# Kernel tuning notes

Hardware: AMD Instinct MI355X
Metric: run time of the kernel (lower is better)

The kernel has to match this reference:

```python
import math
import jax, jax.numpy as jnp
import numpy as np

B, S, D, H = 2, 2048, 1024, 16
DH = D // H


def setup_inputs() -> dict:
    key = jax.random.key(0)
    ks = jax.random.split(key, 12)
    s = 1.0 / math.sqrt(D)
    return {
        "x_q": jax.random.normal(ks[0], (B, S, D), jnp.float32),
        "x_k": jax.random.normal(ks[1], (B, S, D), jnp.float32),
        "x_v": jax.random.normal(ks[2], (B, S, D), jnp.float32),
        "mask": jax.random.randint(ks[3], (B, S), 0, 2) > 0,
        "Wq": jax.random.normal(ks[4], (D, D), jnp.float32) * s,
        "bq": jnp.zeros((D,), jnp.float32),
        "Wk": jax.random.normal(ks[5], (D, D), jnp.float32) * s,
        "bk": jnp.zeros((D,), jnp.float32),
        "Wv": jax.random.normal(ks[6], (D, D), jnp.float32) * s,
        "bv": jnp.zeros((D,), jnp.float32),
        "Wo": jax.random.normal(ks[7], (D, D), jnp.float32) * s,
        "bo": jnp.zeros((D,), jnp.float32),
    }


def reference(x_q, x_k, x_v, mask, Wq, bq, Wk, bk, Wv, bv, Wo, bo):
    # nn.Linear: y = x @ W^T + b
    Q = jnp.einsum('bsd,ed->bse', x_q, Wq) + bq
    K = jnp.einsum('bsd,ed->bse', x_k, Wk) + bk
    V = jnp.einsum('bsd,ed->bse', x_v, Wv) + bv
    b, sq, d = Q.shape
    # split(dim_split, 2) + cat(dim=0) == per-head attention on [B,S,H,DH]
    Qh = Q.reshape(b, sq, H, DH)
    Kh = K.reshape(b, -1, H, DH)
    Vh = V.reshape(b, -1, H, DH)
    scores = jnp.einsum('bqhd,bkhd->bhqk', Qh, Kh) / math.sqrt(DH)
    # inf_mask: -1e9 where mask is False, broadcast over heads and queries
    scores = scores + jnp.where(mask[:, None, None, :], 0.0, -1e9)
    A = jax.nn.softmax(scores, axis=-1)  # dropout is identity in eval
    out = jnp.einsum('bhqk,bkhd->bqhd', A, Vh).reshape(b, sq, d)
    return jnp.einsum('bsd,ed->bse', out, Wo) + bo
```

## Files before the change

### kernel.cpp

```cpp
#include <hip/hip_runtime.h>
#include <hip/hip_bf16.h>
#include <stdint.h>

#define BB  2
#define SS  2048
#define DDIM 1024
#define HH  16
#define DH  64

typedef __attribute__((ext_vector_type(8))) short short8;
typedef __attribute__((ext_vector_type(4))) short short4v;
typedef __attribute__((ext_vector_type(4))) float float4v;

#define AS1 __attribute__((address_space(1)))
#define AS3 __attribute__((address_space(3)))

static __device__ __forceinline__ void gl2lds16(const void* g, void* l) {
  __builtin_amdgcn_global_load_lds((const AS1 unsigned int*)g,
                                   (AS3 unsigned int*)l, 16, 0, 0);
}

static __device__ __forceinline__ float bf2f(short s) {
  union { unsigned u; float f; } c;
  c.u = ((unsigned)(unsigned short)s) << 16;
  return c.f;
}
static __device__ __forceinline__ short f2bf(float f) {
  union { float ff; unsigned u; } c;
  c.ff = f;
  unsigned u = c.u;
  u += 0x7fffu + ((u >> 16) & 1u);
  return (short)(u >> 16);
}

static __device__ __forceinline__ unsigned cvtpk(float x, float y) {
  union { __hip_bfloat162 h; unsigned u; } c;
  c.h = __float22bfloat162_rn(float2{x, y});
  return c.u;
}

#if __has_builtin(__builtin_amdgcn_exp2f)
static __device__ __forceinline__ float exp2fast(float x) { return __builtin_amdgcn_exp2f(x); }
#else
static __device__ __forceinline__ float exp2fast(float x) { return __expf(x * 0.69314718056f); }
#endif

static __device__ __forceinline__ int detect_f32(const void* p) {
  const float* f = (const float*)p;
  int ok = 1;
#pragma unroll
  for (int i = 0; i < 16; i++) {
    float a = fabsf(f[i]);
    ok &= (a > 1e-10f && a < 1e4f) ? 1 : 0;
  }
  return ok;
}

struct CvtArgs {
  const void* xq; const void* xk; const void* xv;
  const void* wq; const void* wk; const void* wv; const void* wo;
  const void* b0; const void* b1; const void* b2; const void* b3;
  const int* mask;
  short* dst;
  float* mw;
};

__global__ __launch_bounds__(256)
void cvt_kernel(CvtArgs a) {
  const int f32m = detect_f32(a.xq);
  const size_t gtid = (size_t)blockIdx.x * blockDim.x + threadIdx.x;
  const size_t stride = (size_t)gridDim.x * blockDim.x;
  const size_t M4 = (size_t)4 << 20, M1 = (size_t)1 << 20, TOT = (size_t)16 << 20;
  for (size_t i = gtid; i * 4 < TOT; i += stride) {
    const size_t idx = i * 4;
    const void* src;
    size_t off;
    if (idx < 3 * M4) {
      size_t xi = idx / M4;
      off = idx & (M4 - 1);
      src = (xi == 0) ? a.xq : (xi == 1) ? a.xk : a.xv;
    } else {
      size_t wi = (idx - 3 * M4) / M1;
      off = idx & (M1 - 1);
      src = (wi == 0) ? a.wq : (wi == 1) ? a.wk : (wi == 2) ? a.wv : a.wo;
    }
    short4v o;
    if (f32m) {
      float4v v = *(const float4v*)((const float*)src + off);
      union { unsigned u[2]; short4v s; } pk;
      pk.u[0] = cvtpk(v[0], v[1]);
      pk.u[1] = cvtpk(v[2], v[3]);
      o = pk.s;
    } else {
      o = *(const short4v*)((const short*)src + off);
    }
    *(short4v*)(a.dst + idx) = o;
  }
  if (gtid < 1024) {
    const void* bs[4] = {a.b0, a.b1, a.b2, a.b3};
#pragma unroll
    for (int j = 0; j < 4; j++) {
      short v = f32m ? f2bf(((const float*)bs[j])[gtid])
                     : ((const short*)bs[j])[gtid];
      a.dst[TOT + (size_t)j * 1024 + gtid] = v;
    }
  }
  if (gtid < BB * SS)
    a.mw[gtid] = a.mask[gtid] ? -23.083120654223414f : -1e9f;
}

struct GemmArgs {
  const short* x[3];
  const short* w[3];
  const short* b[3];
  short* o[3];
  const void* probe;
  int tmask;
  int detect_out;
};

template <int MW>
__global__ __launch_bounds__(256)
void gemm_kernel(GemmArgs a) {
  constexpr int GK = 1024, GN = 1024;
  __shared__ alignas(16) short As[32 * MW * 32];
  __shared__ alignas(16) short Bs[128 * 32];

  const int t = threadIdx.x;
  const int w = t >> 6, l = t & 63, l15 = l & 15, qd = l >> 4;
  const int bn = blockIdx.x, bm = blockIdx.y, mat = blockIdx.z;

  const short* X  = a.x[mat];
  const short* W  = a.w[mat];
  const short* Bi = a.b[mat];
  short* O        = a.o[mat];
  const int transposed = (a.tmask >> mat) & 1;

  const short* Ag = X + (size_t)bm * (32 * MW) * GK;
  const short* Bg = W + (size_t)bn * 128 * GK;

  const int L0 = t, L1 = 256 + t;
  const int r0 = L0 >> 2, g0 = (L0 & 3) ^ ((r0 >> 1) & 3);
  const int r1 = L1 >> 2, g1 = (L1 & 3) ^ ((r1 >> 1) & 3);
  const size_t off0 = (size_t)r0 * GK + g0 * 8;
  const size_t off1 = (size_t)r1 * GK + g1 * 8;

  float4v acc[MW][4];
#pragma unroll
  for (int i = 0; i < MW; i++)
#pragma unroll
    for (int j = 0; j < 4; j++) acc[i][j] = (float4v){0.f, 0.f, 0.f, 0.f};

  const int wm = (w >> 1) * 16 * MW, wn = (w & 1) * 64;

  for (int k0 = 0; k0 < GK; k0 += 32) {
    gl2lds16(Ag + off0 + k0, (char*)As + L0 * 16);
    if (MW == 4) gl2lds16(Ag + off1 + k0, (char*)As + L1 * 16);
    gl2lds16(Bg + off0 + k0, (char*)Bs + L0 * 16);
    gl2lds16(Bg + off1 + k0, (char*)Bs + L1 * 16);
    __syncthreads();

    short8 af[MW], bf[4];
#pragma unroll
    for (int i = 0; i < MW; i++) {
      int m = wm + i * 16 + l15;
      af[i] = *(const short8*)((const char*)As + (m * 4 + (qd ^ ((m >> 1) & 3))) * 16);
    }
#pragma unroll
    for (int j = 0; j < 4; j++) {
      int n = wn + j * 16 + l15;
      bf[j] = *(const short8*)((const char*)Bs + (n * 4 + (qd ^ ((n >> 1) & 3))) * 16);
    }
#pragma unroll
    for (int i = 0; i < MW; i++)
#pragma unroll
      for (int j = 0; j < 4; j++)
        acc[i][j] = __builtin_amdgcn_mfma_f32_16x16x32_bf16(af[i], bf[j], acc[i][j], 0, 0, 0);
    __syncthreads();
  }

  if (!transposed) {
    const int outf32 = a.detect_out ? detect_f32(a.probe) : 0;
    float bj[4];
#pragma unroll
    for (int j = 0; j < 4; j++) bj[j] = bf2f(Bi[bn * 128 + wn + j * 16 + l15]);
#pragma unroll
    for (int i = 0; i < MW; i++) {
      int mgl = bm * (32 * MW) + wm + i * 16 + qd * 4;
#pragma unroll
      for (int j = 0; j < 4; j++) {
        int ngl = bn * 128 + wn + j * 16 + l15;
        if (outf32) {
          float* Of = (float*)O;
#pragma unroll
          for (int r = 0; r < 4; r++)
            Of[(size_t)(mgl + r) * GN + ngl] = acc[i][j][r] + bj[j];
        } else {
#pragma unroll
          for (int r = 0; r < 4; r++)
            O[(size_t)(mgl + r) * GN + ngl] = f2bf(acc[i][j][r] + bj[j]);
        }
      }
    }
  } else {
#pragma unroll
    for (int j = 0; j < 4; j++) {
      int ngl = bn * 128 + wn + j * 16 + l15;
      float bb = bf2f(Bi[ngl]);
#pragma unroll
      for (int i = 0; i < MW; i++) {
        int mgl = bm * (32 * MW) + wm + i * 16 + qd * 4;
        int bidx = mgl >> 11;
        int s = mgl & (SS - 1);
        short4v v;
#pragma unroll
        for (int r = 0; r < 4; r++) v[r] = f2bf(acc[i][j][r] + bb);
        *(short4v*)(O + (size_t)bidx * DDIM * SS + (size_t)ngl * SS + s) = v;
      }
    }
  }
}

__global__ __launch_bounds__(128)
void flash_kernel(const short* __restrict__ Q, const short* __restrict__ K,
                  const short* __restrict__ Vt, const float* __restrict__ Mw,
                  short* __restrict__ At) {
  __shared__ alignas(16) short Ks[2][64 * 64];
  __shared__ alignas(16) short Vs[2][64 * 64];

  const int t = threadIdx.x;
  const int w = t >> 6, l = t & 63, l15 = l & 15, qd = l >> 4;
  const int x = blockIdx.x;
  const int bh = x & 31, qt = x >> 5;
  const int b = bh >> 4, h = bh & 15;
  const int q0 = qt * 64 + w * 32;

  const float SC = 0.125f * 1.44269504f;

  short8 qf[2][2];
#pragma unroll
  for (int g = 0; g < 2; g++) {
    const short* Qb = Q + ((size_t)(b * SS + q0 + 16 * g + l15)) * DDIM + h * 64;
#pragma unroll
    for (int c = 0; c < 2; c++) qf[g][c] = *(const short8*)(Qb + 32 * c + 8 * qd);
  }

  const short ov = (l15 == 0) ? (short)0x3F80 : (short)0;
  const short8 onesf = {ov, ov, ov, ov, ov, ov, ov, ov};

  const int kr = t >> 3;
  const int kc = (t & 7) ^ (kr & 7);
  int pk[4];
#pragma unroll
  for (int c = 0; c < 4; c++)
    pk[c] = ((c >> 1) << 5) | ((kr >> 2) << 3) | ((c & 1) << 2) | (kr & 3);
  const short* KgB = K + (size_t)(b * SS) * DDIM + h * 64 + kc * 8;
  const short* VgB = Vt + (size_t)b * DDIM * SS + (size_t)(h * 64 + kr) * SS + kc * 8;
  const float* MwB = Mw + b * SS;

  float4v oacc[2][4], oaccl[2];
#pragma unroll
  for (int g = 0; g < 2; g++) {
    oaccl[g] = (float4v){0.f, 0.f, 0.f, 0.f};
#pragma unroll
    for (int mt = 0; mt < 4; mt++) oacc[g][mt] = (float4v){0.f, 0.f, 0.f, 0.f};
  }

  const int swz = l15 & 7;

#pragma unroll
  for (int c = 0; c < 4; c++)
    gl2lds16(KgB + (size_t)pk[c] * DDIM, (char*)Ks[0] + c * 2048 + t * 16);
#pragma unroll
  for (int c = 0; c < 4; c++)
    gl2lds16(VgB + (size_t)(16 * c) * SS, (char*)Vs[0] + c * 2048 + t * 16);

  for (int i = 0; i < 32; i++) {
    const int cur = i & 1, nxt = cur ^ 1;
    asm volatile("s_waitcnt vmcnt(0)\n\ts_barrier" ::: "memory");

    if (i < 31) {
      const size_t ko = (size_t)((i + 1) * 64) * DDIM;
      const int vo = (i + 1) * 64;
#pragma unroll
      for (int c = 0; c < 4; c++)
        gl2lds16(KgB + ko + (size_t)pk[c] * DDIM, (char*)Ks[nxt] + c * 2048 + t * 16);
#pragma unroll
      for (int c = 0; c < 4; c++)
        gl2lds16(VgB + vo + (size_t)(16 * c) * SS, (char*)Vs[nxt] + c * 2048 + t * 16);
    }

    float4v ma[2][2];
#pragma unroll
    for (int pp = 0; pp < 2; pp++)
#pragma unroll
      for (int s = 0; s < 2; s++)
        ma[pp][s] = *(const float4v*)(MwB + i * 64 + 32 * pp + 8 * qd + 4 * s);

    const short* ksb = Ks[cur];
    const short* vsb = Vs[cur];

    float4v sacc[2][4];
#pragma unroll
    for (int g = 0; g < 2; g++)
#pragma unroll
      for (int mt = 0; mt < 4; mt++) sacc[g][mt] = (float4v){0.f, 0.f, 0.f, 0.f};
#pragma unroll
    for (int mt = 0; mt < 4; mt++) {
#pragma unroll
      for (int c = 0; c < 2; c++) {
        short8 kf = *(const short8*)(ksb + (mt * 16 + l15) * 64 + (((4 * c + qd) ^ swz) * 8));
#pragma unroll
        for (int g = 0; g < 2; g++)
          sacc[g][mt] = __builtin_amdgcn_mfma_f32_16x16x32_bf16(kf, qf[g][c], sacc[g][mt], 0, 0, 0);
      }
    }

#pragma unroll
    for (int pp = 0; pp < 2; pp++) {
      short8 vf[4];
#pragma unroll
      for (int mt = 0; mt < 4; mt++)
        vf[mt] = *(const short8*)(vsb + (mt * 16 + l15) * 64 + (((4 * pp + qd) ^ swz) * 8));
#pragma unroll
      for (int g = 0; g < 2; g++) {
        float p0[4], p1[4];
#pragma unroll
        for (int r = 0; r < 4; r++) {
          p0[r] = exp2fast(fmaf(sacc[g][2 * pp][r],     SC, ma[pp][0][r]));
          p1[r] = exp2fast(fmaf(sacc[g][2 * pp + 1][r], SC, ma[pp][1][r]));
        }
        union { unsigned u[4]; short8 v8; } pkk;
        pkk.u[0] = cvtpk(p0[0], p0[1]);
        pkk.u[1] = cvtpk(p0[2], p0[3]);
        pkk.u[2] = cvtpk(p1[0], p1[1]);
        pkk.u[3] = cvtpk(p1[2], p1[3]);
#pragma unroll
        for (int mt = 0; mt < 4; mt++)
          oacc[g][mt] = __builtin_amdgcn_mfma_f32_16x16x32_bf16(vf[mt], pkk.v8, oacc[g][mt], 0, 0, 0);
        oaccl[g] = __builtin_amdgcn_mfma_f32_16x16x32_bf16(onesf, pkk.v8, oaccl[g], 0, 0, 0);
      }
    }
  }

#pragma unroll
  for (int g = 0; g < 2; g++) {
    const float lg = __shfl(oaccl[g][0], l15);
    const float inv = 1.f / lg;
    short* Og = At + ((size_t)(b * SS + q0 + 16 * g + l15)) * DDIM + h * 64;
#pragma unroll
    for (int mt = 0; mt < 4; mt++) {
      short4v v;
#pragma unroll
      for (int r = 0; r < 4; r++) v[r] = f2bf(oacc[g][mt][r] * inv);
      *(short4v*)(Og + mt * 16 + qd * 4) = v;
    }
  }
}

extern "C" void kernel_launch(void* const* d_in, const int* in_sizes, int n_in,
                              void* d_out, int out_size, void* d_ws, size_t ws_size,
                              hipStream_t stream) {
  (void)in_sizes; (void)n_in; (void)out_size; (void)ws_size;
  const int* mask = (const int*)d_in[3];

  char* ws = (char*)d_ws;
  short* wsBF = (short*)ws;
  const size_t M1 = (size_t)1 << 20;
  short* Qb = (short*)(ws + (size_t)34 * M1);
  short* Kb = (short*)(ws + (size_t)42 * M1);
  short* Vt = (short*)(ws + (size_t)50 * M1);
  short* At = (short*)(ws + (size_t)58 * M1);
  float* Mw = (float*)(ws + (size_t)66 * M1);

  CvtArgs c;
  c.xq = d_in[0]; c.xk = d_in[1]; c.xv = d_in[2];
  c.wq = d_in[4]; c.wk = d_in[6]; c.wv = d_in[8]; c.wo = d_in[10];
  c.b0 = d_in[5]; c.b1 = d_in[7]; c.b2 = d_in[9]; c.b3 = d_in[11];
  c.mask = mask; c.dst = wsBF; c.mw = Mw;
  hipLaunchKernelGGL(cvt_kernel, dim3(4096), dim3(256), 0, stream, c);

  GemmArgs a1;
  a1.x[0] = wsBF;            a1.x[1] = wsBF + 4 * M1;  a1.x[2] = wsBF + 8 * M1;
  a1.w[0] = wsBF + 12 * M1;  a1.w[1] = wsBF + 13 * M1; a1.w[2] = wsBF + 14 * M1;
  a1.b[0] = wsBF + 16 * M1;  a1.b[1] = wsBF + 16 * M1 + 1024;
  a1.b[2] = wsBF + 16 * M1 + 2048;
  a1.o[0] = Qb; a1.o[1] = Kb; a1.o[2] = Vt;
  a1.probe = d_in[0];
  a1.tmask = 4;
  a1.detect_out = 0;
  hipLaunchKernelGGL(HIP_KERNEL_NAME(gemm_kernel<4>), dim3(8, 32, 3), dim3(256),
                     0, stream, a1);

  hipLaunchKernelGGL(flash_kernel, dim3(1024), dim3(128), 0, stream,
                     Qb, Kb, Vt, Mw, At);

  GemmArgs a2;
  a2.x[0] = At;             a2.w[0] = wsBF + 15 * M1;
  a2.b[0] = wsBF + 16 * M1 + 3072;
  a2.o[0] = (short*)d_out;
  a2.x[1] = a2.x[2] = At; a2.w[1] = a2.w[2] = a2.w[0];
  a2.b[1] = a2.b[2] = a2.b[0]; a2.o[1] = a2.o[2] = a2.o[0];
  a2.probe = d_in[0];
  a2.tmask = 0;
  a2.detect_out = 1;
  hipLaunchKernelGGL(HIP_KERNEL_NAME(gemm_kernel<2>), dim3(8, 64, 1), dim3(256),
                     0, stream, a2);
}
```

Baseline: 249.8 us.

## Double GEMM K-step and enlarge flash attention tiles to 128 queries and keys

The GEMM kernel now stages 64-wide K slices per barrier instead of 32, using a new 8-chunk XOR swizzle, which halves the number of sync rounds. The flash kernel grows to 4 waves covering 128 queries per block and loads 128-key K/V tiles per iteration, processed in two halves. Each K/V tile is now shared by twice as many queries and there are fewer barriers. In exchange LDS use rises (flash is now 64KB double-buffered) and fewer blocks are launched, which may lower occupancy.

```diff
diff --git a/kernel.cpp b/kernel.cpp
--- a/kernel.cpp
+++ b/kernel.cpp
@@ -123,8 +123,8 @@
 __global__ __launch_bounds__(256)
 void gemm_kernel(GemmArgs a) {
   constexpr int GK = 1024, GN = 1024;
-  __shared__ alignas(16) short As[32 * MW * 32];
-  __shared__ alignas(16) short Bs[128 * 32];
+  __shared__ alignas(16) short As[32 * MW * 64];
+  __shared__ alignas(16) short Bs[128 * 64];
 
   const int t = threadIdx.x;
   const int w = t >> 6, l = t & 63, l15 = l & 15, qd = l >> 4;
@@ -139,11 +139,8 @@
   const short* Ag = X + (size_t)bm * (32 * MW) * GK;
   const short* Bg = W + (size_t)bn * 128 * GK;
 
-  const int L0 = t, L1 = 256 + t;
-  const int r0 = L0 >> 2, g0 = (L0 & 3) ^ ((r0 >> 1) & 3);
-  const int r1 = L1 >> 2, g1 = (L1 & 3) ^ ((r1 >> 1) & 3);
-  const size_t off0 = (size_t)r0 * GK + g0 * 8;
-  const size_t off1 = (size_t)r1 * GK + g1 * 8;
+  const int sr = t >> 3, sc = t & 7;
+  const int schk = (sc ^ (sr & 7)) * 8;
 
   float4v acc[MW][4];
 #pragma unroll
@@ -152,30 +149,40 @@
     for (int j = 0; j < 4; j++) acc[i][j] = (float4v){0.f, 0.f, 0.f, 0.f};
 
   const int wm = (w >> 1) * 16 * MW, wn = (w & 1) * 64;
-
-  for (int k0 = 0; k0 < GK; k0 += 32) {
-    gl2lds16(Ag + off0 + k0, (char*)As + L0 * 16);
-    if (MW == 4) gl2lds16(Ag + off1 + k0, (char*)As + L1 * 16);
-    gl2lds16(Bg + off0 + k0, (char*)Bs + L0 * 16);
-    gl2lds16(Bg + off1 + k0, (char*)Bs + L1 * 16);
+  const int swz = l15 & 7;
+
+  for (int k0 = 0; k0 < GK; k0 += 64) {
+#pragma unroll
+    for (int c = 0; c < MW; c++) {
+      int r = 32 * c + sr;
+      gl2lds16(Ag + (size_t)r * GK + k0 + schk, (char*)As + (r * 8 + sc) * 16);
+    }
+#pragma unroll
+    for (int c = 0; c < 4; c++) {
+      int r = 32 * c + sr;
+      gl2lds16(Bg + (size_t)r * GK + k0 + schk, (char*)Bs + (r * 8 + sc) * 16);
+    }
     __syncthreads();
 
-    short8 af[MW], bf[4];
-#pragma unroll
-    for (int i = 0; i < MW; i++) {
-      int m = wm + i * 16 + l15;
-      af[i] = *(const short8*)((const char*)As + (m * 4 + (qd ^ ((m >> 1) & 3))) * 16);
-    }
-#pragma unroll
-    for (int j = 0; j < 4; j++) {
-      int n = wn + j * 16 + l15;
-      bf[j] = *(const short8*)((const char*)Bs + (n * 4 + (qd ^ ((n >> 1) & 3))) * 16);
-    }
-#pragma unroll
-    for (int i = 0; i < MW; i++)
-#pragma unroll
-      for (int j = 0; j < 4; j++)
-        acc[i][j] = __builtin_amdgcn_mfma_f32_16x16x32_bf16(af[i], bf[j], acc[i][j], 0, 0, 0);
+#pragma unroll
+    for (int ks = 0; ks < 2; ks++) {
+      short8 af[MW], bf[4];
+#pragma unroll
+      for (int i = 0; i < MW; i++) {
+        int m = wm + i * 16 + l15;
+        af[i] = *(const short8*)((const char*)As + (m * 8 + ((ks * 4 + qd) ^ swz)) * 16);
+      }
+#pragma unroll
+      for (int j = 0; j < 4; j++) {
+        int n = wn + j * 16 + l15;
+        bf[j] = *(const short8*)((const char*)Bs + (n * 8 + ((ks * 4 + qd) ^ swz)) * 16);
+      }
+#pragma unroll
+      for (int i = 0; i < MW; i++)
+#pragma unroll
+        for (int j = 0; j < 4; j++)
+          acc[i][j] = __builtin_amdgcn_mfma_f32_16x16x32_bf16(af[i], bf[j], acc[i][j], 0, 0, 0);
+    }
     __syncthreads();
   }
 
@@ -221,19 +228,18 @@
   }
 }
 
-__global__ __launch_bounds__(128)
+__global__ __launch_bounds__(256)
 void flash_kernel(const short* __restrict__ Q, const short* __restrict__ K,
                   const short* __restrict__ Vt, const float* __restrict__ Mw,
                   short* __restrict__ At) {
-  __shared__ alignas(16) short Ks[2][64 * 64];
-  __shared__ alignas(16) short Vs[2][64 * 64];
+  __shared__ alignas(16) short Ks[2][128 * 64];
+  __shared__ alignas(16) short Vs[2][64 * 128];
 
   const int t = threadIdx.x;
   const int w = t >> 6, l = t & 63, l15 = l & 15, qd = l >> 4;
-  const int x = blockIdx.x;
-  const int bh = x & 31, qt = x >> 5;
+  const int bh = blockIdx.x, qt = blockIdx.y;
   const int b = bh >> 4, h = bh & 15;
-  const int q0 = qt * 64 + w * 32;
+  const int q0 = qt * 128 + w * 32;
 
   const float SC = 0.125f * 1.44269504f;
 
@@ -248,14 +254,19 @@
   const short ov = (l15 == 0) ? (short)0x3F80 : (short)0;
   const short8 onesf = {ov, ov, ov, ov, ov, ov, ov, ov};
 
-  const int kr = t >> 3;
-  const int kc = (t & 7) ^ (kr & 7);
-  int pk[4];
-#pragma unroll
-  for (int c = 0; c < 4; c++)
-    pk[c] = ((c >> 1) << 5) | ((kr >> 2) << 3) | ((c & 1) << 2) | (kr & 3);
-  const short* KgB = K + (size_t)(b * SS) * DDIM + h * 64 + kc * 8;
-  const short* VgB = Vt + (size_t)b * DDIM * SS + (size_t)(h * 64 + kr) * SS + kc * 8;
+  const int sr = t >> 3, sc8 = t & 7;
+  const int kchk = ((sc8 ^ (sr & 7)) * 8);
+  int pkey[4];
+#pragma unroll
+  for (int c = 0; c < 4; c++) {
+    int r = 32 * c + sr, L = r & 63;
+    pkey[c] = (r & 64) | ((L >> 5) << 5) | (((L >> 2) & 3) << 3)
+              | (((L >> 4) & 1) << 2) | (L & 3);
+  }
+  const short* KgB = K + (size_t)(b * SS) * DDIM + h * 64 + kchk;
+  const int vr = t >> 4, vc = t & 15;
+  const short* VgB = Vt + (size_t)b * DDIM * SS + (size_t)(h * 64 + vr) * SS
+                     + ((vc ^ (vr & 7)) * 8);
   const float* MwB = Mw + b * SS;
 
   float4v oacc[2][4], oaccl[2];
@@ -270,75 +281,85 @@
 
 #pragma unroll
   for (int c = 0; c < 4; c++)
-    gl2lds16(KgB + (size_t)pk[c] * DDIM, (char*)Ks[0] + c * 2048 + t * 16);
+    gl2lds16(KgB + (size_t)pkey[c] * DDIM, (char*)Ks[0] + (c * 256 + 64 * w + l) * 16);
 #pragma unroll
   for (int c = 0; c < 4; c++)
-    gl2lds16(VgB + (size_t)(16 * c) * SS, (char*)Vs[0] + c * 2048 + t * 16);
-
-  for (int i = 0; i < 32; i++) {
+    gl2lds16(VgB + 16 * c * SS, (char*)Vs[0] + (c * 256 + 64 * w + l) * 16);
+
+  for (int i = 0; i < 16; i++) {
     const int cur = i & 1, nxt = cur ^ 1;
     asm volatile("s_waitcnt vmcnt(0)\n\ts_barrier" ::: "memory");
 
-    if (i < 31) {
-      const size_t ko = (size_t)((i + 1) * 64) * DDIM;
-      const int vo = (i + 1) * 64;
+    if (i < 15) {
+      const size_t ko = (size_t)((i + 1) * 128) * DDIM;
+      const int vo = (i + 1) * 128;
 #pragma unroll
       for (int c = 0; c < 4; c++)
-        gl2lds16(KgB + ko + (size_t)pk[c] * DDIM, (char*)Ks[nxt] + c * 2048 + t * 16);
+        gl2lds16(KgB + ko + (size_t)pkey[c] * DDIM,
+                 (char*)Ks[nxt] + (c * 256 + 64 * w + l) * 16);
 #pragma unroll
       for (int c = 0; c < 4; c++)
-        gl2lds16(VgB + vo + (size_t)(16 * c) * SS, (char*)Vs[nxt] + c * 2048 + t * 16);
-    }
-
-    float4v ma[2][2];
-#pragma unroll
-    for (int pp = 0; pp < 2; pp++)
-#pragma unroll
-      for (int s = 0; s < 2; s++)
-        ma[pp][s] = *(const float4v*)(MwB + i * 64 + 32 * pp + 8 * qd + 4 * s);
+        gl2lds16(VgB + vo + 16 * c * SS,
+                 (char*)Vs[nxt] + (c * 256 + 64 * w + l) * 16);
+    }
 
     const short* ksb = Ks[cur];
     const short* vsb = Vs[cur];
 
-    float4v sacc[2][4];
-#pragma unroll
-    for (int g = 0; g < 2; g++)
-#pragma unroll
-      for (int mt = 0; mt < 4; mt++) sacc[g][mt] = (float4v){0.f, 0.f, 0.f, 0.f};
-#pragma unroll
-    for (int mt = 0; mt < 4; mt++) {
-#pragma unroll
-      for (int c = 0; c < 2; c++) {
-        short8 kf = *(const short8*)(ksb + (mt * 16 + l15) * 64 + (((4 * c + qd) ^ swz) * 8));
-#pragma unroll
-        for (int g = 0; g < 2; g++)
-          sacc[g][mt] = __builtin_amdgcn_mfma_f32_16x16x32_bf16(kf, qf[g][c], sacc[g][mt], 0, 0, 0);
-      }
-    }
-
-#pragma unroll
-    for (int pp = 0; pp < 2; pp++) {
-      short8 vf[4];
-#pragma unroll
-      for (int mt = 0; mt < 4; mt++)
-        vf[mt] = *(const short8*)(vsb + (mt * 16 + l15) * 64 + (((4 * pp + qd) ^ swz) * 8));
-#pragma unroll
-      for (int g = 0; g < 2; g++) {
-        float p0[4], p1[4];
-#pragma unroll
-        for (int r = 0; r < 4; r++) {
-          p0[r] = exp2fast(fmaf(sacc[g][2 * pp][r],     SC, ma[pp][0][r]));
-          p1[r] = exp2fast(fmaf(sacc[g][2 * pp + 1][r], SC, ma[pp][1][r]));
+#pragma unroll
+    for (int half = 0; half < 2; half++) {
+      float4v sacc[2][4];
+#pragma unroll
+      for (int g = 0; g < 2; g++)
+#pragma unroll
+        for (int mt = 0; mt < 4; mt++) sacc[g][mt] = (float4v){0.f, 0.f, 0.f, 0.f};
+#pragma unroll
+      for (int mt = 0; mt < 4; mt++) {
+#pragma unroll
+        for (int c = 0; c < 2; c++) {
+          short8 kf = *(const short8*)(ksb + (half * 64 + mt * 16 + l15) * 64
+                                       + (((4 * c + qd) ^ swz) * 8));
+#pragma unroll
+          for (int g = 0; g < 2; g++)
+            sacc[g][mt] = __builtin_amdgcn_mfma_f32_16x16x32_bf16(kf, qf[g][c], sacc[g][mt], 0, 0, 0);
         }
-        union { unsigned u[4]; short8 v8; } pkk;
-        pkk.u[0] = cvtpk(p0[0], p0[1]);
-        pkk.u[1] = cvtpk(p0[2], p0[3]);
-        pkk.u[2] = cvtpk(p1[0], p1[1]);
-        pkk.u[3] = cvtpk(p1[2], p1[3]);
-#pragma unroll
-        for (int mt = 0; mt < 4; mt++)
-          oacc[g][mt] = __builtin_amdgcn_mfma_f32_16x16x32_bf16(vf[mt], pkk.v8, oacc[g][mt], 0, 0, 0);
-        oaccl[g] = __builtin_amdgcn_mfma_f32_16x16x32_bf16(onesf, pkk.v8, oaccl[g], 0, 0, 0);
+      }
+
+      float4v ma[2][2];
+#pragma unroll
+      for (int pp = 0; pp < 2; pp++)
+#pragma unroll
+        for (int s = 0; s < 2; s++)
+          ma[pp][s] = *(const float4v*)(MwB + i * 128 + half * 64 + 32 * pp
+                                        + 8 * qd + 4 * s);
+
+#pragma unroll
+      for (int pp = 0; pp < 2; pp++) {
+        short8 vf[4];
+#pragma unroll
+        for (int mt = 0; mt < 4; mt++) {
+          const int row = mt * 16 + l15;
+          const int chunk = (8 * half + 4 * pp + qd) ^ swz;
+          vf[mt] = *(const short8*)(vsb + row * 128 + chunk * 8);
+        }
+#pragma unroll
+        for (int g = 0; g < 2; g++) {
+          float p0[4], p1[4];
+#pragma unroll
+          for (int r = 0; r < 4; r++) {
+            p0[r] = exp2fast(fmaf(sacc[g][2 * pp][r],     SC, ma[pp][0][r]));
+            p1[r] = exp2fast(fmaf(sacc[g][2 * pp + 1][r], SC, ma[pp][1][r]));
+          }
+          union { unsigned u[4]; short8 v8; } pkk;
+          pkk.u[0] = cvtpk(p0[0], p0[1]);
+          pkk.u[1] = cvtpk(p0[2], p0[3]);
+          pkk.u[2] = cvtpk(p1[0], p1[1]);
+          pkk.u[3] = cvtpk(p1[2], p1[3]);
+#pragma unroll
+          for (int mt = 0; mt < 4; mt++)
+            oacc[g][mt] = __builtin_amdgcn_mfma_f32_16x16x32_bf16(vf[mt], pkk.v8, oacc[g][mt], 0, 0, 0);
+          oaccl[g] = __builtin_amdgcn_mfma_f32_16x16x32_bf16(onesf, pkk.v8, oaccl[g], 0, 0, 0);
+        }
       }
     }
   }
@@ -392,7 +413,7 @@
   hipLaunchKernelGGL(HIP_KERNEL_NAME(gemm_kernel<4>), dim3(8, 32, 3), dim3(256),
                      0, stream, a1);
 
-  hipLaunchKernelGGL(flash_kernel, dim3(1024), dim3(128), 0, stream,
+  hipLaunchKernelGGL(flash_kernel, dim3(32, 16), dim3(256), 0, stream,
                      Qb, Kb, Vt, Mw, At);
 
   GemmArgs a2;
```

Result: faster. 243.2 us (-2.6%).
